# Performance work log

Hardware: AMD Instinct MI355X
Metric: run time of the kernel (lower is better)

Reference implementation:

```python
import jax, jax.numpy as jnp
import numpy as np

N, E, H, EF = 50000, 800000, 128, 32
MSG_IN = 2 * H + EF + 3  # 291
UPD_IN = 2 * H           # 256


def _mlp(x, W1, b1, W2, b2):
    # Linear -> ReLU -> Linear (act=True: ReLU between layers)
    h = jax.nn.relu(x @ W1 + b1)
    return h @ W2 + b2


def _layernorm(x, gamma, beta, eps=1e-5):
    mu = jnp.mean(x, axis=-1, keepdims=True)
    var = jnp.var(x, axis=-1, keepdims=True)
    return (x - mu) * jax.lax.rsqrt(var + eps) * gamma + beta


def setup_inputs() -> dict:
    key = jax.random.key(0)
    ks = jax.random.split(key, 12)
    def w(k, shape):
        fan_in = shape[0]
        return jax.random.uniform(k, shape, jnp.float32, -1.0, 1.0) / np.sqrt(fan_in)
    return {
        "x": jax.random.normal(ks[0], (N, H), jnp.float32),
        "edge_index": jax.random.randint(ks[1], (2, E), 0, N, jnp.int32),
        "edge_attr": jax.random.normal(ks[2], (E, EF), jnp.float32),
        "coords": jax.random.normal(ks[3], (N, 3), jnp.float32),
        "mW1": w(ks[4], (MSG_IN, H)), "mb1": jnp.zeros((H,), jnp.float32),
        "mW2": w(ks[5], (H, H)),      "mb2": jnp.zeros((H,), jnp.float32),
        "uW1": w(ks[6], (UPD_IN, H)), "ub1": jnp.zeros((H,), jnp.float32),
        "uW2": w(ks[7], (H, H)),      "ub2": jnp.zeros((H,), jnp.float32),
        "gamma": jnp.ones((H,), jnp.float32),
        "beta": jnp.zeros((H,), jnp.float32),
    }


def reference(x, edge_index, edge_attr, coords,
              mW1, mb1, mW2, mb2, uW1, ub1, uW2, ub2, gamma, beta):
    src, dst = edge_index[0], edge_index[1]
    rel_coords = coords[dst] - coords[src]                       # (E, 3)
    msg_input = jnp.concatenate([x[src], x[dst], edge_attr, rel_coords], axis=-1)  # (E, MSG_IN)
    messages = _mlp(msg_input, mW1, mb1, mW2, mb2)               # (E, H)
    aggr = jax.ops.segment_sum(messages, dst, num_segments=x.shape[0])  # (N, H)
    update_input = jnp.concatenate([x, aggr], axis=-1)           # (N, 2H)
    out = _mlp(update_input, uW1, ub1, uW2, ub2)                 # (N, H)
    return _layernorm(x + out, gamma, beta)
```

## Files before the change

kernel.cpp:

```cpp
#include <hip/hip_runtime.h>

#define NN 50000
#define NE 800000
#define HD 128

typedef short short8 __attribute__((ext_vector_type(8)));
typedef float floatx4 __attribute__((ext_vector_type(4)));
typedef float floatx16 __attribute__((ext_vector_type(16)));

static __device__ __forceinline__ unsigned short f2bf(float f) {
    unsigned int u = __float_as_uint(f);
    unsigned int lsb = (u >> 16) & 1u;
    u += 0x7fffu + lsb;
    return (unsigned short)(u >> 16);
}

static __device__ __forceinline__ short8 pack2(float4 a, float4 b) {
    union { unsigned int u[4]; short8 s; } r;
    asm("v_cvt_pk_bf16_f32 %0, %1, %2" : "=v"(r.u[0]) : "v"(a.x), "v"(a.y));
    asm("v_cvt_pk_bf16_f32 %0, %1, %2" : "=v"(r.u[1]) : "v"(a.z), "v"(a.w));
    asm("v_cvt_pk_bf16_f32 %0, %1, %2" : "=v"(r.u[2]) : "v"(b.x), "v"(b.y));
    asm("v_cvt_pk_bf16_f32 %0, %1, %2" : "=v"(r.u[3]) : "v"(b.z), "v"(b.w));
    return r.s;
}

static __device__ __forceinline__ floatx4 mfma16x16x32(short8 a, short8 b, floatx4 c) {
    asm("v_mfma_f32_16x16x32_bf16 %0, %1, %2, %0" : "+v"(c) : "v"(a), "v"(b));
    return c;
}

static __device__ __forceinline__ floatx16 mfma32x32x16(short8 a, short8 b, floatx16 c) {
    asm("v_mfma_f32_32x32x16_bf16 %0, %1, %2, %0" : "+v"(c) : "v"(a), "v"(b));
    return c;
}

#define NOPGUARD_INIT8(A) asm volatile("s_nop 3" \
  : "+v"(A[0]),"+v"(A[1]),"+v"(A[2]),"+v"(A[3]),"+v"(A[4]),"+v"(A[5]),"+v"(A[6]),"+v"(A[7]))
#define NOPGUARD8(A) asm volatile("s_nop 7\ns_nop 7" \
  : "+v"(A[0]),"+v"(A[1]),"+v"(A[2]),"+v"(A[3]),"+v"(A[4]),"+v"(A[5]),"+v"(A[6]),"+v"(A[7]))
#define NOPGUARD_INIT4x16(A) asm volatile("s_nop 7" \
  : "+v"(A[0]),"+v"(A[1]),"+v"(A[2]),"+v"(A[3]))
#define NOPGUARD4x16(A) asm volatile("s_nop 7\ns_nop 7\ns_nop 7" \
  : "+v"(A[0]),"+v"(A[1]),"+v"(A[2]),"+v"(A[3]))

#define WAVE_LDS_FENCE() asm volatile("s_waitcnt lgkmcnt(0)" ::: "memory")

__global__ void pack_weights(const float* __restrict__ mW1, const float* __restrict__ mW2,
                             const float* __restrict__ uW1, const float* __restrict__ uW2,
                             unsigned short* __restrict__ W1q, unsigned short* __restrict__ W2q,
                             unsigned short* __restrict__ U1p, unsigned short* __restrict__ U2p) {
    int t = blockIdx.x * 256 + threadIdx.x;
    if (t < 40960) {
        int i = t;
        int j = i & 7, lane = (i >> 3) & 63, n = (i >> 9) & 3, s = i >> 11;
        int k = s * 16 + ((lane >> 5) << 3) + j;
        int c = n * 32 + (lane & 31);
        W1q[i] = f2bf((k < 291) ? mW1[k * 128 + c] : 0.0f);
    } else if (t < 57344) {
        int i = t - 40960;
        int j = i & 7, lane = (i >> 3) & 63, n = (i >> 9) & 3, s = i >> 11;
        int k = s * 16 + ((lane >> 5) << 3) + j;
        int c = n * 32 + (lane & 31);
        W2q[i] = f2bf(mW2[k * 128 + c]);
    } else if (t < 90112) {
        int i = t - 57344;
        int j = i & 7, lane = (i >> 3) & 63, n = (i >> 9) & 7, kk = i >> 12;
        int k = kk * 32 + ((lane >> 4) << 3) + j;
        int c = n * 16 + (lane & 15);
        U1p[i] = f2bf(uW1[k * 128 + c]);
    } else if (t < 106496) {
        int i = t - 90112;
        int j = i & 7, lane = (i >> 3) & 63, n = (i >> 9) & 7, kk = i >> 12;
        int k = kk * 32 + ((lane >> 4) << 3) + j;
        int c = n * 16 + (lane & 15);
        U2p[i] = f2bf(uW2[k * 128 + c]);
    }
}

__global__ void cast_kernel(const float* __restrict__ in, unsigned short* __restrict__ out,
                            int n8) {
    int t = blockIdx.x * 256 + threadIdx.x;
    if (t < n8) {
        float4 a = *reinterpret_cast<const float4*>(in + (size_t)t * 8);
        float4 b = *reinterpret_cast<const float4*>(in + (size_t)t * 8 + 4);
        *reinterpret_cast<short8*>(out + (size_t)t * 8) = pack2(a, b);
    }
}

__global__ void hist_kernel(const int* __restrict__ ei, int* __restrict__ counts) {
    int e = blockIdx.x * 256 + threadIdx.x;
    if (e < NE) atomicAdd(&counts[ei[NE + e]], 1);
}

__global__ __launch_bounds__(1024)
void scan1_kernel(const int* __restrict__ counts, int* __restrict__ partial,
                  int* __restrict__ bsum) {
    __shared__ int wsum[16];
    int tid = threadIdx.x;
    int gid = blockIdx.x * 1024 + tid;
    int lane = tid & 63, w = tid >> 6;
    int v = (gid < NN) ? counts[gid] : 0;
    int s = v;
    #pragma unroll
    for (int o = 1; o < 64; o <<= 1) { int t = __shfl_up(s, o); if (lane >= o) s += t; }
    if (lane == 63) wsum[w] = s;
    __syncthreads();
    if (w == 0 && lane < 16) {
        int t = wsum[lane];
        #pragma unroll
        for (int o = 1; o < 16; o <<= 1) { int u = __shfl_up(t, o); if (lane >= o) t += u; }
        wsum[lane] = t;
    }
    __syncthreads();
    int base = (w > 0) ? wsum[w - 1] : 0;
    if (gid < NN) partial[gid] = base + s - v;
    if (tid == 1023) bsum[blockIdx.x] = base + s;
}

__global__ void scan2_kernel(int* __restrict__ bsum, int n) {
    int lane = threadIdx.x;
    int v = (lane < n) ? bsum[lane] : 0;
    int s = v;
    #pragma unroll
    for (int o = 1; o < 64; o <<= 1) { int t = __shfl_up(s, o); if (lane >= o) s += t; }
    if (lane < n) bsum[lane] = s - v;
}

__global__ void scatter_kernel(const int* __restrict__ ei, const int* __restrict__ partial,
                               const int* __restrict__ bsum, int* __restrict__ cursor,
                               const float* __restrict__ cd, const float* __restrict__ ea,
                               unsigned int* __restrict__ epack,
                               uint2* __restrict__ relb,
                               unsigned short* __restrict__ eab) {
    int e = blockIdx.x * 256 + threadIdx.x;
    if (e < NE) {
        int d = ei[NE + e];
        int s = ei[e];
        int pos = partial[d] + bsum[d >> 10] + atomicAdd(&cursor[d], 1);
        epack[pos] = (unsigned int)s | ((unsigned int)d << 16);
        float r0 = cd[d * 3 + 0] - cd[s * 3 + 0];
        float r1 = cd[d * 3 + 1] - cd[s * 3 + 1];
        float r2 = cd[d * 3 + 2] - cd[s * 3 + 2];
        uint2 rr;
        asm("v_cvt_pk_bf16_f32 %0, %1, %2" : "=v"(rr.x) : "v"(r0), "v"(r1));
        asm("v_cvt_pk_bf16_f32 %0, %1, %2" : "=v"(rr.y) : "v"(r2), "v"(0.0f));
        relb[pos] = rr;
        const float* eap = ea + (size_t)e * 32;
        unsigned short* eo = eab + (size_t)pos * 32;
        #pragma unroll
        for (int q = 0; q < 4; ++q) {
            float4 a = *reinterpret_cast<const float4*>(eap + q * 8);
            float4 b = *reinterpret_cast<const float4*>(eap + q * 8 + 4);
            *reinterpret_cast<short8*>(eo + q * 8) = pack2(a, b);
        }
    }
}

__global__ __launch_bounds__(256, 4)
void msg_kernel(const unsigned short* __restrict__ xb, const unsigned short* __restrict__ eab,
                const unsigned int* __restrict__ epack, const uint2* __restrict__ relb,
                const unsigned short* __restrict__ W1q, const float* __restrict__ mb1,
                const unsigned short* __restrict__ W2q, const float* __restrict__ mb2,
                float* __restrict__ aggr) {
    __shared__ unsigned short sH[128 * 136];
    __shared__ int sDst[128];

    const int tid = threadIdx.x;
    const int lane = tid & 63;
    const int wid = tid >> 6;
    const int lr31 = lane & 31;
    const int half = lane >> 5;
    const int wrow = wid * 32 + lr31;
    const int eidx = blockIdx.x * 128 + wrow;

    const unsigned int p = epack[eidx];
    const int src = (int)(p & 0xFFFFu);
    const int dst = (int)(p >> 16);
    if (half == 0) sDst[wrow] = dst;

    const unsigned short* xs = xb + (size_t)src * 128 + half * 8;
    const unsigned short* xd = xb + (size_t)dst * 128 + half * 8;
    const unsigned short* epr = eab + (size_t)eidx * 32 + half * 8;
    const uint2 rr = relb[eidx];

    const short8* w1 = reinterpret_cast<const short8*>(W1q);
    const short8* w2 = reinterpret_cast<const short8*>(W2q);

    floatx16 acc[4];
    #pragma unroll
    for (int n = 0; n < 4; ++n)
        #pragma unroll
        for (int q = 0; q < 16; ++q) acc[n][q] = 0.0f;
    NOPGUARD_INIT4x16(acc);

    #pragma unroll
    for (int s = 0; s < 8; ++s) {
        short8 a = *reinterpret_cast<const short8*>(xs + s * 16);
        const short8* wb = w1 + (s * 4) * 64 + lane;
        #pragma unroll
        for (int n = 0; n < 4; ++n) acc[n] = mfma32x32x16(a, wb[n * 64], acc[n]);
    }
    #pragma unroll
    for (int s = 8; s < 16; ++s) {
        short8 a = *reinterpret_cast<const short8*>(xd + (s - 8) * 16);
        const short8* wb = w1 + (s * 4) * 64 + lane;
        #pragma unroll
        for (int n = 0; n < 4; ++n) acc[n] = mfma32x32x16(a, wb[n * 64], acc[n]);
    }
    #pragma unroll
    for (int s = 16; s < 18; ++s) {
        short8 a = *reinterpret_cast<const short8*>(epr + (s - 16) * 16);
        const short8* wb = w1 + (s * 4) * 64 + lane;
        #pragma unroll
        for (int n = 0; n < 4; ++n) acc[n] = mfma32x32x16(a, wb[n * 64], acc[n]);
    }
    {
        union { unsigned int u[4]; short8 s; } a9;
        a9.u[0] = (half == 0) ? rr.x : 0u;
        a9.u[1] = (half == 0) ? rr.y : 0u;
        a9.u[2] = 0u; a9.u[3] = 0u;
        const short8* wb = w1 + (18 * 4) * 64 + lane;
        #pragma unroll
        for (int n = 0; n < 4; ++n) acc[n] = mfma32x32x16(a9.s, wb[n * 64], acc[n]);
    }
    NOPGUARD4x16(acc);

    WAVE_LDS_FENCE();
    unsigned int hm32;
    {
        bool head = false;
        if (lane < 32) {
            int r = wid * 32 + lane;
            head = (lane == 0) || (sDst[r] != sDst[r - 1]);
        }
        unsigned long long m = __ballot(head);
        hm32 = (unsigned int)(m & 0xFFFFFFFFull);
    }

    #pragma unroll
    for (int n = 0; n < 4; ++n) {
        float bias = mb1[n * 32 + lr31];
        #pragma unroll
        for (int q = 0; q < 16; ++q) {
            int crow = (q & 3) + 8 * (q >> 2) + 4 * half;
            sH[(wid * 32 + crow) * 136 + n * 32 + lr31] = f2bf(fmaxf(acc[n][q] + bias, 0.0f));
        }
    }
    WAVE_LDS_FENCE();

    floatx16 acc2[4];
    #pragma unroll
    for (int n = 0; n < 4; ++n)
        #pragma unroll
        for (int q = 0; q < 16; ++q) acc2[n][q] = 0.0f;
    NOPGUARD_INIT4x16(acc2);

    #pragma unroll
    for (int s = 0; s < 8; ++s) {
        short8 a = *reinterpret_cast<const short8*>(&sH[wrow * 136 + s * 16 + half * 8]);
        const short8* wb = w2 + (s * 4) * 64 + lane;
        #pragma unroll
        for (int n = 0; n < 4; ++n) acc2[n] = mfma32x32x16(a, wb[n * 64], acc2[n]);
    }
    NOPGUARD4x16(acc2);
    WAVE_LDS_FENCE();

    #pragma unroll
    for (int n = 0; n < 4; ++n) {
        float bias = mb2[n * 32 + lr31];
        #pragma unroll
        for (int q = 0; q < 16; ++q) {
            int crow = (q & 3) + 8 * (q >> 2) + 4 * half;
            sH[(wid * 32 + crow) * 136 + n * 32 + lr31] = f2bf(acc2[n][q] + bias);
        }
    }
    WAVE_LDS_FENCE();

    {
        unsigned int m = hm32;
        while (m) {
            int start = __ffs(m) - 1;
            unsigned int m2 = m & (m - 1);
            int end = m2 ? (__ffs(m2) - 1) : 32;
            float sum0 = 0.0f, sum1 = 0.0f;
            for (int r = start; r < end; ++r) {
                int rw = wid * 32 + r;
                unsigned int u0 = sH[rw * 136 + lane];
                unsigned int u1 = sH[rw * 136 + 64 + lane];
                sum0 += __uint_as_float(u0 << 16);
                sum1 += __uint_as_float(u1 << 16);
            }
            int d = sDst[wid * 32 + start];
            atomicAdd(&aggr[d * 128 + lane], sum0);
            atomicAdd(&aggr[d * 128 + 64 + lane], sum1);
            m = m2;
        }
    }
}

__global__
void node_kernel(const unsigned short* __restrict__ xb, const float* __restrict__ x,
                 const float* __restrict__ aggr,
                 const unsigned short* __restrict__ U1p, const float* __restrict__ ub1,
                 const unsigned short* __restrict__ U2p, const float* __restrict__ ub2,
                 const float* __restrict__ gamma, const float* __restrict__ beta,
                 float* __restrict__ out) {
    __shared__ unsigned short sH[64 * 136];

    const int tid = threadIdx.x;
    const int lane = tid & 63;
    const int wid = tid >> 6;
    const int g = lane >> 4;
    const int lr = lane & 15;
    const int arow = wid * 16 + lr;
    const int n0 = blockIdx.x * 64;

    int nd0 = n0 + arow;
    int ndc0 = (nd0 < NN) ? nd0 : (NN - 1);

    const unsigned short* xp = xb + (size_t)ndc0 * 128 + g * 8;
    const float* ap = aggr + (size_t)ndc0 * 128 + g * 8;

    short8 af[8];
    float4 ta[8];
    #pragma unroll
    for (int kk = 0; kk < 4; ++kk) {
        af[kk] = *reinterpret_cast<const short8*>(xp + kk * 32);
        ta[2 * kk]     = *reinterpret_cast<const float4*>(ap + kk * 32);
        ta[2 * kk + 1] = *reinterpret_cast<const float4*>(ap + kk * 32 + 4);
    }
    #pragma unroll
    for (int kk = 0; kk < 4; ++kk)
        af[4 + kk] = pack2(ta[2 * kk], ta[2 * kk + 1]);

    floatx4 acc[8];
    #pragma unroll
    for (int n = 0; n < 8; ++n)
        #pragma unroll
        for (int r = 0; r < 4; ++r) acc[n][r] = 0.0f;
    NOPGUARD_INIT8(acc);

    #pragma unroll
    for (int kk = 0; kk < 8; ++kk) {
        const short8* wb = reinterpret_cast<const short8*>(U1p) + (kk * 8) * 64 + lane;
        #pragma unroll
        for (int n = 0; n < 8; ++n)
            acc[n] = mfma16x16x32(af[kk], wb[n * 64], acc[n]);
    }
    NOPGUARD8(acc);

    #pragma unroll
    for (int n = 0; n < 8; ++n) {
        float bias = ub1[n * 16 + lr];
        #pragma unroll
        for (int r = 0; r < 4; ++r) {
            int row = wid * 16 + g * 4 + r;
            sH[row * 136 + n * 16 + lr] = f2bf(fmaxf(acc[n][r] + bias, 0.0f));
        }
    }
    WAVE_LDS_FENCE();

    short8 a2[4];
    #pragma unroll
    for (int kk = 0; kk < 4; ++kk)
        a2[kk] = *reinterpret_cast<const short8*>(&sH[arow * 136 + kk * 32 + g * 8]);

    floatx4 acc2[8];
    #pragma unroll
    for (int n = 0; n < 8; ++n)
        #pragma unroll
        for (int r = 0; r < 4; ++r) acc2[n][r] = 0.0f;
    NOPGUARD_INIT8(acc2);

    #pragma unroll
    for (int kk = 0; kk < 4; ++kk) {
        const short8* wb = reinterpret_cast<const short8*>(U2p) + (kk * 8) * 64 + lane;
        #pragma unroll
        for (int n = 0; n < 8; ++n)
            acc2[n] = mfma16x16x32(a2[kk], wb[n * 64], acc2[n]);
    }
    NOPGUARD8(acc2);

    #pragma unroll
    for (int r = 0; r < 4; ++r) {
        int row = wid * 16 + g * 4 + r;
        int nd = n0 + row;
        int ndc = (nd < NN) ? nd : (NN - 1);
        float vals[8];
        float s1 = 0.0f, s2 = 0.0f;
        #pragma unroll
        for (int n = 0; n < 8; ++n) {
            int col = n * 16 + lr;
            float v = acc2[n][r] + ub2[col] + x[ndc * 128 + col];
            vals[n] = v;
            s1 += v;
            s2 += v * v;
        }
        #pragma unroll
        for (int m = 1; m < 16; m <<= 1) {
            s1 += __shfl_xor(s1, m);
            s2 += __shfl_xor(s2, m);
        }
        float mean = s1 * (1.0f / 128.0f);
        float var = s2 * (1.0f / 128.0f) - mean * mean;
        float inv = rsqrtf(var + 1e-5f);
        if (nd < NN) {
            #pragma unroll
            for (int n = 0; n < 8; ++n) {
                int col = n * 16 + lr;
                out[nd * 128 + col] = (vals[n] - mean) * inv * gamma[col] + beta[col];
            }
        }
    }
}

extern "C" void kernel_launch(void* const* d_in, const int* in_sizes, int n_in,
                              void* d_out, int out_size, void* d_ws, size_t ws_size,
                              hipStream_t stream) {
    const float* x     = (const float*)d_in[0];
    const int*   ei    = (const int*)d_in[1];
    const float* ea    = (const float*)d_in[2];
    const float* cd    = (const float*)d_in[3];
    const float* mW1   = (const float*)d_in[4];
    const float* mb1   = (const float*)d_in[5];
    const float* mW2   = (const float*)d_in[6];
    const float* mb2   = (const float*)d_in[7];
    const float* uW1   = (const float*)d_in[8];
    const float* ub1   = (const float*)d_in[9];
    const float* uW2   = (const float*)d_in[10];
    const float* ub2   = (const float*)d_in[11];
    const float* gamma = (const float*)d_in[12];
    const float* beta  = (const float*)d_in[13];
    float* out = (float*)d_out;

    char* ws = (char*)d_ws;
    unsigned short* W1q = (unsigned short*)(ws);
    unsigned short* W2q = (unsigned short*)(ws + 81920);
    unsigned short* U1p = (unsigned short*)(ws + 114688);
    unsigned short* U2p = (unsigned short*)(ws + 180224);
    int* counts  = (int*)(ws + 212992);
    int* cursor  = (int*)(ws + 413696);
    int* partial = (int*)(ws + 614400);
    int* bsum    = (int*)(ws + 815104);
    unsigned int* epack = (unsigned int*)(ws + 815360);
    uint2* relb  = (uint2*)(ws + 4015360);
    unsigned short* xbuf = (unsigned short*)(ws + 10415360);
    unsigned short* eabuf = (unsigned short*)(ws + 23215360);

    float* aggr = out;

    hipMemsetAsync(counts, 0, (size_t)(614400 - 212992), stream);
    hipMemsetAsync(aggr, 0, (size_t)NN * HD * sizeof(float), stream);

    pack_weights<<<416, 256, 0, stream>>>(mW1, mW2, uW1, uW2, W1q, W2q, U1p, U2p);
    cast_kernel<<<(NN * HD / 8 + 255) / 256, 256, 0, stream>>>(x, xbuf, NN * HD / 8);
    hist_kernel<<<(NE + 255) / 256, 256, 0, stream>>>(ei, counts);
    scan1_kernel<<<(NN + 1023) / 1024, 1024, 0, stream>>>(counts, partial, bsum);
    scan2_kernel<<<1, 64, 0, stream>>>(bsum, (NN + 1023) / 1024);
    scatter_kernel<<<(NE + 255) / 256, 256, 0, stream>>>(ei, partial, bsum, cursor, cd, ea, epack, relb, eabuf);
    msg_kernel<<<NE / 128, 256, 0, stream>>>(xbuf, eabuf, epack, relb, W1q, mb1, W2q, mb2, aggr);
    node_kernel<<<(NN + 63) / 64, 256, 0, stream>>>(xbuf, x, aggr, U1p, ub1, U2p, ub2, gamma, beta, out);
}
```

Measured before the change: 285.5 us.

## Pair waves to share 64-edge tiles, splitting output columns between waves

Each pair of waves now handles 64 edges. Each wave computes half of the 128 output columns for two 32-row tiles, so every loaded weight fragment is reused across two A tiles and each gathered A fragment feeds two MFMAs. This halves weight reads from global memory or cache per MFMA. In exchange, every wave gathers rows for 64 edges, and the waves in a pair must coordinate through block-wide __syncthreads. Segment detection and the atomic scatter now span 64 rows, which can reduce the number of atomics per destination segment.

```diff
diff --git a/kernel.cpp b/kernel.cpp
--- a/kernel.cpp
+++ b/kernel.cpp
@@ -165,134 +165,146 @@
     __shared__ unsigned short sH[128 * 136];
     __shared__ int sDst[128];
 
-    const int tid = threadIdx.x;
+    const int tid  = threadIdx.x;
     const int lane = tid & 63;
-    const int wid = tid >> 6;
+    const int wid  = tid >> 6;
     const int lr31 = lane & 31;
     const int half = lane >> 5;
-    const int wrow = wid * 32 + lr31;
-    const int eidx = blockIdx.x * 128 + wrow;
-
-    const unsigned int p = epack[eidx];
-    const int src = (int)(p & 0xFFFFu);
-    const int dst = (int)(p >> 16);
-    if (half == 0) sDst[wrow] = dst;
-
-    const unsigned short* xs = xb + (size_t)src * 128 + half * 8;
-    const unsigned short* xd = xb + (size_t)dst * 128 + half * 8;
-    const unsigned short* epr = eab + (size_t)eidx * 32 + half * 8;
-    const uint2 rr = relb[eidx];
+    const int pair = wid >> 1;
+    const int pw   = wid & 1;
+    const int prow0 = pair * 64;
+    const int ebase = blockIdx.x * 128 + prow0;
+
+    const unsigned short* xs[2];
+    const unsigned short* xd[2];
+    const unsigned short* epr[2];
+    uint2 rr[2];
+    #pragma unroll
+    for (int t = 0; t < 2; ++t) {
+        int er = t * 32 + lr31;
+        unsigned int p = epack[ebase + er];
+        int src = (int)(p & 0xFFFFu);
+        int dst = (int)(p >> 16);
+        if (pw == 0 && half == 0) sDst[prow0 + er] = dst;
+        xs[t]  = xb + (size_t)src * 128 + half * 8;
+        xd[t]  = xb + (size_t)dst * 128 + half * 8;
+        epr[t] = eab + (size_t)(ebase + er) * 32 + half * 8;
+        rr[t]  = relb[ebase + er];
+    }
 
     const short8* w1 = reinterpret_cast<const short8*>(W1q);
     const short8* w2 = reinterpret_cast<const short8*>(W2q);
 
     floatx16 acc[4];
     #pragma unroll
-    for (int n = 0; n < 4; ++n)
-        #pragma unroll
-        for (int q = 0; q < 16; ++q) acc[n][q] = 0.0f;
+    for (int i = 0; i < 4; ++i)
+        #pragma unroll
+        for (int q = 0; q < 16; ++q) acc[i][q] = 0.0f;
     NOPGUARD_INIT4x16(acc);
 
     #pragma unroll
+    for (int s = 0; s < 19; ++s) {
+        short8 a0, a1;
+        if (s < 8) {
+            a0 = *reinterpret_cast<const short8*>(xs[0] + s * 16);
+            a1 = *reinterpret_cast<const short8*>(xs[1] + s * 16);
+        } else if (s < 16) {
+            a0 = *reinterpret_cast<const short8*>(xd[0] + (s - 8) * 16);
+            a1 = *reinterpret_cast<const short8*>(xd[1] + (s - 8) * 16);
+        } else if (s < 18) {
+            a0 = *reinterpret_cast<const short8*>(epr[0] + (s - 16) * 16);
+            a1 = *reinterpret_cast<const short8*>(epr[1] + (s - 16) * 16);
+        } else {
+            union { unsigned int u[4]; short8 s8; } z0, z1;
+            z0.u[0] = (half == 0) ? rr[0].x : 0u;
+            z0.u[1] = (half == 0) ? rr[0].y : 0u;
+            z0.u[2] = 0u; z0.u[3] = 0u;
+            z1.u[0] = (half == 0) ? rr[1].x : 0u;
+            z1.u[1] = (half == 0) ? rr[1].y : 0u;
+            z1.u[2] = 0u; z1.u[3] = 0u;
+            a0 = z0.s8; a1 = z1.s8;
+        }
+        const short8* wb = w1 + (s * 4 + pw * 2) * 64 + lane;
+        short8 b0 = wb[0];
+        short8 b1 = wb[64];
+        acc[0] = mfma32x32x16(a0, b0, acc[0]);
+        acc[1] = mfma32x32x16(a0, b1, acc[1]);
+        acc[2] = mfma32x32x16(a1, b0, acc[2]);
+        acc[3] = mfma32x32x16(a1, b1, acc[3]);
+    }
+    NOPGUARD4x16(acc);
+
+    #pragma unroll
+    for (int t = 0; t < 2; ++t)
+        #pragma unroll
+        for (int n = 0; n < 2; ++n) {
+            int col = pw * 64 + n * 32 + lr31;
+            float bias = mb1[col];
+            #pragma unroll
+            for (int q = 0; q < 16; ++q) {
+                int crow = (q & 3) + 8 * (q >> 2) + 4 * half;
+                sH[(prow0 + t * 32 + crow) * 136 + col] =
+                    f2bf(fmaxf(acc[t * 2 + n][q] + bias, 0.0f));
+            }
+        }
+    __syncthreads();
+
+    unsigned long long hm;
+    {
+        int r = prow0 + lane;
+        bool head = (lane == 0) || (sDst[r] != sDst[r - 1]);
+        hm = __ballot(head);
+    }
+
+    floatx16 acc2[4];
+    #pragma unroll
+    for (int i = 0; i < 4; ++i)
+        #pragma unroll
+        for (int q = 0; q < 16; ++q) acc2[i][q] = 0.0f;
+    NOPGUARD_INIT4x16(acc2);
+
+    #pragma unroll
     for (int s = 0; s < 8; ++s) {
-        short8 a = *reinterpret_cast<const short8*>(xs + s * 16);
-        const short8* wb = w1 + (s * 4) * 64 + lane;
-        #pragma unroll
-        for (int n = 0; n < 4; ++n) acc[n] = mfma32x32x16(a, wb[n * 64], acc[n]);
-    }
-    #pragma unroll
-    for (int s = 8; s < 16; ++s) {
-        short8 a = *reinterpret_cast<const short8*>(xd + (s - 8) * 16);
-        const short8* wb = w1 + (s * 4) * 64 + lane;
-        #pragma unroll
-        for (int n = 0; n < 4; ++n) acc[n] = mfma32x32x16(a, wb[n * 64], acc[n]);
-    }
-    #pragma unroll
-    for (int s = 16; s < 18; ++s) {
-        short8 a = *reinterpret_cast<const short8*>(epr + (s - 16) * 16);
-        const short8* wb = w1 + (s * 4) * 64 + lane;
-        #pragma unroll
-        for (int n = 0; n < 4; ++n) acc[n] = mfma32x32x16(a, wb[n * 64], acc[n]);
-    }
+        short8 a0 = *reinterpret_cast<const short8*>(&sH[(prow0 + lr31) * 136 + s * 16 + half * 8]);
+        short8 a1 = *reinterpret_cast<const short8*>(&sH[(prow0 + 32 + lr31) * 136 + s * 16 + half * 8]);
+        const short8* wb = w2 + (s * 4 + pw * 2) * 64 + lane;
+        short8 b0 = wb[0];
+        short8 b1 = wb[64];
+        acc2[0] = mfma32x32x16(a0, b0, acc2[0]);
+        acc2[1] = mfma32x32x16(a0, b1, acc2[1]);
+        acc2[2] = mfma32x32x16(a1, b0, acc2[2]);
+        acc2[3] = mfma32x32x16(a1, b1, acc2[3]);
+    }
+    NOPGUARD4x16(acc2);
+    __syncthreads();
+
+    #pragma unroll
+    for (int t = 0; t < 2; ++t)
+        #pragma unroll
+        for (int n = 0; n < 2; ++n) {
+            int col = pw * 64 + n * 32 + lr31;
+            float bias = mb2[col];
+            #pragma unroll
+            for (int q = 0; q < 16; ++q) {
+                int crow = (q & 3) + 8 * (q >> 2) + 4 * half;
+                sH[(prow0 + t * 32 + crow) * 136 + col] = f2bf(acc2[t * 2 + n][q] + bias);
+            }
+        }
+    WAVE_LDS_FENCE();
+
     {
-        union { unsigned int u[4]; short8 s; } a9;
-        a9.u[0] = (half == 0) ? rr.x : 0u;
-        a9.u[1] = (half == 0) ? rr.y : 0u;
-        a9.u[2] = 0u; a9.u[3] = 0u;
-        const short8* wb = w1 + (18 * 4) * 64 + lane;
-        #pragma unroll
-        for (int n = 0; n < 4; ++n) acc[n] = mfma32x32x16(a9.s, wb[n * 64], acc[n]);
-    }
-    NOPGUARD4x16(acc);
-
-    WAVE_LDS_FENCE();
-    unsigned int hm32;
-    {
-        bool head = false;
-        if (lane < 32) {
-            int r = wid * 32 + lane;
-            head = (lane == 0) || (sDst[r] != sDst[r - 1]);
-        }
-        unsigned long long m = __ballot(head);
-        hm32 = (unsigned int)(m & 0xFFFFFFFFull);
-    }
-
-    #pragma unroll
-    for (int n = 0; n < 4; ++n) {
-        float bias = mb1[n * 32 + lr31];
-        #pragma unroll
-        for (int q = 0; q < 16; ++q) {
-            int crow = (q & 3) + 8 * (q >> 2) + 4 * half;
-            sH[(wid * 32 + crow) * 136 + n * 32 + lr31] = f2bf(fmaxf(acc[n][q] + bias, 0.0f));
-        }
-    }
-    WAVE_LDS_FENCE();
-
-    floatx16 acc2[4];
-    #pragma unroll
-    for (int n = 0; n < 4; ++n)
-        #pragma unroll
-        for (int q = 0; q < 16; ++q) acc2[n][q] = 0.0f;
-    NOPGUARD_INIT4x16(acc2);
-
-    #pragma unroll
-    for (int s = 0; s < 8; ++s) {
-        short8 a = *reinterpret_cast<const short8*>(&sH[wrow * 136 + s * 16 + half * 8]);
-        const short8* wb = w2 + (s * 4) * 64 + lane;
-        #pragma unroll
-        for (int n = 0; n < 4; ++n) acc2[n] = mfma32x32x16(a, wb[n * 64], acc2[n]);
-    }
-    NOPGUARD4x16(acc2);
-    WAVE_LDS_FENCE();
-
-    #pragma unroll
-    for (int n = 0; n < 4; ++n) {
-        float bias = mb2[n * 32 + lr31];
-        #pragma unroll
-        for (int q = 0; q < 16; ++q) {
-            int crow = (q & 3) + 8 * (q >> 2) + 4 * half;
-            sH[(wid * 32 + crow) * 136 + n * 32 + lr31] = f2bf(acc2[n][q] + bias);
-        }
-    }
-    WAVE_LDS_FENCE();
-
-    {
-        unsigned int m = hm32;
+        const int col = pw * 64 + lane;
+        unsigned long long m = hm;
         while (m) {
-            int start = __ffs(m) - 1;
-            unsigned int m2 = m & (m - 1);
-            int end = m2 ? (__ffs(m2) - 1) : 32;
-            float sum0 = 0.0f, sum1 = 0.0f;
+            int start = __ffsll((long long)m) - 1;
+            unsigned long long m2 = m & (m - 1);
+            int end = m2 ? (__ffsll((long long)m2) - 1) : 64;
+            float sum = 0.0f;
             for (int r = start; r < end; ++r) {
-                int rw = wid * 32 + r;
-                unsigned int u0 = sH[rw * 136 + lane];
-                unsigned int u1 = sH[rw * 136 + 64 + lane];
-                sum0 += __uint_as_float(u0 << 16);
-                sum1 += __uint_as_float(u1 << 16);
+                unsigned int u0 = sH[(prow0 + r) * 136 + col];
+                sum += __uint_as_float(u0 << 16);
             }
-            int d = sDst[wid * 32 + start];
-            atomicAdd(&aggr[d * 128 + lane], sum0);
-            atomicAdd(&aggr[d * 128 + 64 + lane], sum1);
+            atomicAdd(&aggr[sDst[prow0 + start] * 128 + col], sum);
             m = m2;
         }
     }
```

New measurement: 323.6 us. 1.13x slower.
